# Performance work log

Hardware: AMD Instinct MI355X
Metric: run time of the kernel (lower is better)

## Reference

```python
import jax, jax.numpy as jnp
import numpy as np
from jax import lax

B, S, H, E, P, K, R = 64, 512, 768, 32, 16, 9, 6
HEADS, C1, C2 = 4, 128, 64
FEAT = 4 * C2 + 1  # e1, e2, e1*e2, context (64 each) + log-distance


def _ln(x, g, b):
    m = x.mean(-1, keepdims=True)
    v = ((x - m) ** 2).mean(-1, keepdims=True)
    return (x - m) * lax.rsqrt(v + 1e-5) * g + b


def _gat(x, adj, W, a_s, a_d, bias, heads, cout, concat):
    # Dense GATConv over a small fully-masked entity graph. adj[b,i,j]=edge j->i (incl. self-loops).
    h = jnp.einsum('bef,fhc->behc', x, W.reshape(x.shape[-1], heads, cout))
    s = jnp.einsum('behc,hc->bhe', h, a_s)  # source-node attention term
    d = jnp.einsum('behc,hc->bhe', h, a_d)  # target-node attention term
    logits = jax.nn.leaky_relu(d[:, :, :, None] + s[:, :, None, :], 0.2)  # [b,h,i,j]
    logits = jnp.where(adj[:, None, :, :], logits, -1e9)
    att = jax.nn.softmax(logits, axis=-1)
    out = jnp.einsum('bhij,bjhc->bihc', att, h)
    out = out.reshape(out.shape[0], out.shape[1], heads * cout) if concat else out.mean(2)
    return out + bias


def _crf_nll(em, tags, mask, start, end, trans):
    # torchcrf: loss = -mean log-likelihood. em [B,S,K]; tags [B,S]; mask [B,S] bool.
    emt = jnp.transpose(em, (1, 0, 2))
    tgt = tags.T
    mkt = mask.T.astype(em.dtype)
    num0 = start[tgt[0]] + jnp.take_along_axis(emt[0], tgt[0][:, None], 1)[:, 0]

    def nstep(c, inp):
        ptag, sc = c
        e, t, m = inp
        step = trans[ptag, t] + jnp.take_along_axis(e, t[:, None], 1)[:, 0]
        return (jnp.where(m > 0, t, ptag), sc + step * m), None

    (ltag, num), _ = lax.scan(nstep, (tgt[0], num0), (emt[1:], tgt[1:], mkt[1:]))
    num = num + end[ltag]
    a0 = start[None, :] + emt[0]

    def dstep(a, inp):
        e, m = inp
        nxt = jax.scipy.special.logsumexp(a[:, :, None] + trans[None] + e[:, None, :], axis=1)
        return jnp.where(m[:, None] > 0, nxt, a), None

    aT, _ = lax.scan(dstep, a0, (emt[1:], mkt[1:]))
    Z = jax.scipy.special.logsumexp(aT + end[None], axis=1)
    return jnp.mean(Z - num)


def setup_inputs() -> dict:
    key = jax.random.key(0)
    ks = jax.random.split(key, 24)
    n = lambda i, shape, s=0.05: jax.random.normal(ks[i], shape, jnp.float32) * s
    return {
        'sequence_output': jax.random.normal(ks[0], (B, S, H), jnp.float32),
        'attention_mask': jnp.ones((B, S), jnp.int32),
        'ner_labels': jax.random.randint(ks[1], (B, S), 0, K),
        'entity_start': jax.random.randint(ks[2], (B, E), 0, S - 8),
        'entity_len': jax.random.randint(ks[3], (B, E), 0, 8),
        'pair_e1': jax.random.randint(ks[4], (B, P), 0, E),
        'pair_e2': jax.random.randint(ks[5], (B, P), 0, E),
        'pair_labels': jax.random.randint(ks[6], (B, P), 0, 2),
        'adj_mask': jnp.ones((B, E, E), bool),
        'w_ner1': n(7, (H, 256)), 'b_ner1': jnp.zeros((256,), jnp.float32),
        'w_ner2': n(8, (256, K)), 'b_ner2': jnp.zeros((K,), jnp.float32),
        'crf_start': n(9, (K,), 0.1), 'crf_end': n(10, (K,), 0.1), 'crf_trans': n(11, (K, K), 0.1),
        'w_gat1': n(12, (H, HEADS * C1)), 'a_src1': n(13, (HEADS, C1)), 'a_dst1': n(14, (HEADS, C1)),
        'b_gat1': jnp.zeros((HEADS * C1,), jnp.float32),
        'w_gat2': n(15, (HEADS * C1, C2)), 'a_src2': n(16, (1, C2)), 'a_dst2': n(17, (1, C2)),
        'b_gat2': jnp.zeros((C2,), jnp.float32),
        'w_fe': n(18, (FEAT, 512)), 'b_fe': jnp.zeros((512,), jnp.float32),
        'g_fe': jnp.ones((512,), jnp.float32), 'be_fe': jnp.zeros((512,), jnp.float32),
        'w_rc1': n(19, (R, 512, 256)), 'b_rc1': jnp.zeros((R, 256), jnp.float32),
        'g_rc': jnp.ones((R, 256), jnp.float32), 'be_rc': jnp.zeros((R, 256), jnp.float32),
        'w_rc2': n(20, (R, 256, 1)), 'b_rc2': jnp.zeros((R,), jnp.float32),
    }


def reference(sequence_output, attention_mask, ner_labels, entity_start, entity_len,
              pair_e1, pair_e2, pair_labels, adj_mask,
              w_ner1, b_ner1, w_ner2, b_ner2, crf_start, crf_end, crf_trans,
              w_gat1, a_src1, a_dst1, b_gat1, w_gat2, a_src2, a_dst2, b_gat2,
              w_fe, b_fe, g_fe, be_fe, w_rc1, b_rc1, g_rc, be_rc, w_rc2, b_rc2):
    # NER head (dropout off / eval)
    ner_logits = jnp.maximum(sequence_output @ w_ner1 + b_ner1, 0.0) @ w_ner2 + b_ner2
    ner_loss = _crf_nll(ner_logits, ner_labels, attention_mask.astype(bool),
                        crf_start, crf_end, crf_trans)
    # entity span mean-pool via inclusive cumsum trick
    cs = jnp.concatenate([jnp.zeros((B, 1, H), sequence_output.dtype),
                          jnp.cumsum(sequence_output, axis=1)], axis=1)
    e_end = jnp.clip(entity_start + entity_len, 0, S - 1)
    seg = (jnp.take_along_axis(cs, (e_end + 1)[:, :, None], 1)
           - jnp.take_along_axis(cs, entity_start[:, :, None], 1))
    ent = seg / (e_end - entity_start + 1).astype(sequence_output.dtype)[:, :, None]  # [B,E,H]
    x = _gat(ent, adj_mask, w_gat1, a_src1, a_dst1, b_gat1, HEADS, C1, True)
    x = jnp.maximum(x, 0.0)
    x = _gat(x, adj_mask, w_gat2, a_src2, a_dst2, b_gat2, 1, C2, False)  # [B,E,64]
    x1 = jnp.take_along_axis(x, pair_e1[:, :, None], 1)
    x2 = jnp.take_along_axis(x, pair_e2[:, :, None], 1)
    ctx = jnp.broadcast_to(x.mean(1, keepdims=True), (B, P, C2))
    dist = jnp.log(jnp.abs(pair_e1 - pair_e2).astype(x.dtype) + 1.0)[:, :, None]
    pf = jnp.concatenate([x1, x2, x1 * x2, ctx, dist], axis=-1)  # [B,P,257]
    fe = jax.nn.leaky_relu(_ln(pf @ w_fe + b_fe, g_fe, be_fe), 0.01)
    h1 = jnp.einsum('bpf,rfo->rbpo', fe, w_rc1) + b_rc1[:, None, None, :]
    h1 = jax.nn.leaky_relu(_ln(h1, g_rc[:, None, None, :], be_rc[:, None, None, :]), 0.01)
    z = jnp.einsum('rbpo,ro->rbp', h1, w_rc2[:, :, 0]) + b_rc2[:, None, None]
    y = pair_labels.astype(z.dtype)[None]
    # BCEWithLogitsLoss(pos_weight=2.0), mean per relation type, summed over types
    bce = -(2.0 * y * jax.nn.log_sigmoid(z) + (1.0 - y) * jax.nn.log_sigmoid(-z))
    rel_loss = bce.mean(axis=(1, 2)).sum()
    total = ner_loss + rel_loss
    return ner_logits, z, total
```

## Files before the change

kernel.cpp:

```cpp
#include <hip/hip_runtime.h>
#include <math.h>


#define NB 64
#define NS 512
#define NH 768
#define NE 32
#define NP 16
#define NK 9
#define NR 6
#define NHEADS 4
#define NC1 128
#define NC2 64
#define SEGS 16
#define SEGLEN 32

#define ZOFF 294912
#define TOTOFF 301056

#define WS_ENT   0u
#define WS_X1    2621440u
#define WS_X2    3801088u
#define WS_PF    3956736u
#define WS_FE    4222976u
#define WS_CRF   4747264u
#define WS_REL   4747328u
#define WS_W1T   4747392u
#define WS_WRT   0u
#define WS_WFET  393216u
#define WS_SEG   475136u

typedef __attribute__((ext_vector_type(8))) short bf16x8;
typedef __attribute__((ext_vector_type(4))) float f32x4;

__device__ __forceinline__ unsigned short f2bf(float x) {
  union { float f; unsigned u; } v; v.f = x;
  unsigned r = v.u + 0x7FFFu + ((v.u >> 16) & 1u);
  return (unsigned short)(r >> 16);
}

__device__ __forceinline__ float logsigf(float x) {
  if (x >= 0.f) return -log1pf(__expf(-x));
  return x - log1pf(__expf(x));
}

__global__ __launch_bounds__(256) void k_w1t(const float* __restrict__ w1,
    unsigned short* __restrict__ w1t) {
  __shared__ unsigned short tr[32 * 776];
  const int c0 = blockIdx.x * 32;
  const int t = threadIdx.x;
#pragma unroll
  for (int p = 0; p < 24; p++) {
    const int k = p * 32 + (t >> 3), c4 = t & 7;
    const float4 f = *reinterpret_cast<const float4*>(&w1[(size_t)k * 256 + c0 + c4 * 4]);
    tr[(c4 * 4 + 0) * 776 + k] = f2bf(f.x);
    tr[(c4 * 4 + 1) * 776 + k] = f2bf(f.y);
    tr[(c4 * 4 + 2) * 776 + k] = f2bf(f.z);
    tr[(c4 * 4 + 3) * 776 + k] = f2bf(f.w);
  }
  __syncthreads();
  const int c = t >> 3, q = t & 7;
#pragma unroll
  for (int i = 0; i < 12; i++) {
    *reinterpret_cast<uint4*>(&w1t[(size_t)(c0 + c) * NH + q * 96 + i * 8]) =
        *reinterpret_cast<const uint4*>(&tr[c * 776 + q * 96 + i * 8]);
  }
}

__global__ __launch_bounds__(256) void k_wconv(const float* __restrict__ wrc,
    const float* __restrict__ wfe, unsigned short* __restrict__ wrt,
    unsigned short* __restrict__ wfet) {
  __shared__ unsigned short tr[256 * 72];
  const int t = threadIdx.x;
  if (blockIdx.x < 48) {
    const int r = blockIdx.x >> 3, kt = blockIdx.x & 7;
    const int k0 = kt * 64;
#pragma unroll
    for (int i = 0; i < 16; i++) {
      const int slot = t + 256 * i;
      const int row = slot >> 6, c4 = slot & 63;
      const float4 f = *reinterpret_cast<const float4*>(
          &wrc[((size_t)(r * 512) + k0 + row) * 256 + c4 * 4]);
      tr[(c4 * 4 + 0) * 72 + row] = f2bf(f.x);
      tr[(c4 * 4 + 1) * 72 + row] = f2bf(f.y);
      tr[(c4 * 4 + 2) * 72 + row] = f2bf(f.z);
      tr[(c4 * 4 + 3) * 72 + row] = f2bf(f.w);
    }
    __syncthreads();
#pragma unroll
    for (int i = 0; i < 8; i++) {
      const int slot = t + 256 * i;
      const int col = slot >> 3, q = slot & 7;
      *reinterpret_cast<uint4*>(&wrt[((size_t)(r * 256 + col)) * 512 + k0 + q * 8]) =
          *reinterpret_cast<const uint4*>(&tr[col * 72 + q * 8]);
    }
  } else {
    const int bid = blockIdx.x - 48;
    const int kt = bid % 5, cb = bid / 5;
    const int k0 = kt * 64, c0 = cb * 256;
#pragma unroll
    for (int i = 0; i < 16; i++) {
      const int slot = t + 256 * i;
      const int row = slot >> 6, c4 = slot & 63;
      const int k = k0 + row;
      float4 f = {0.f, 0.f, 0.f, 0.f};
      if (k < 257)
        f = *reinterpret_cast<const float4*>(&wfe[(size_t)k * 512 + c0 + c4 * 4]);
      tr[(c4 * 4 + 0) * 72 + row] = f2bf(f.x);
      tr[(c4 * 4 + 1) * 72 + row] = f2bf(f.y);
      tr[(c4 * 4 + 2) * 72 + row] = f2bf(f.z);
      tr[(c4 * 4 + 3) * 72 + row] = f2bf(f.w);
    }
    __syncthreads();
#pragma unroll
    for (int i = 0; i < 8; i++) {
      const int slot = t + 256 * i;
      const int col = slot >> 3, q = slot & 7;
      *reinterpret_cast<uint4*>(&wfet[((size_t)(c0 + col)) * 320 + k0 + q * 8]) =
          *reinterpret_cast<const uint4*>(&tr[col * 72 + q * 8]);
    }
  }
}

__global__ __launch_bounds__(256) void k_ner(const float* __restrict__ seq,
    const unsigned short* __restrict__ w1t, const float* __restrict__ b1,
    const float* __restrict__ w2, const float* __restrict__ b2,
    float* __restrict__ out) {
  __shared__ unsigned short AsS[64 * 40];
  __shared__ unsigned short BsS[256 * 40];
  __shared__ float zs[64 * 4 * 12];
  const int t = threadIdx.x;
  const int tok0 = blockIdx.x * 64;
  const int w = t >> 6, lane = t & 63, quad = lane >> 4, l15 = lane & 15;

  f32x4 acc[4][4];
#pragma unroll
  for (int r = 0; r < 4; r++)
#pragma unroll
    for (int c = 0; c < 4; c++) acc[r][c] = (f32x4){0.f, 0.f, 0.f, 0.f};

  const int tokA = t >> 2, koffA = (t & 3) * 8;
  const float* aptr = seq + (size_t)(tok0 + tokA) * NH + koffA;

  for (int kt = 0; kt < NH; kt += 32) {
    __syncthreads();
    {
      const float4 f0 = *reinterpret_cast<const float4*>(aptr + kt);
      const float4 f1 = *reinterpret_cast<const float4*>(aptr + kt + 4);
      bf16x8 av;
      av[0] = (short)f2bf(f0.x); av[1] = (short)f2bf(f0.y);
      av[2] = (short)f2bf(f0.z); av[3] = (short)f2bf(f0.w);
      av[4] = (short)f2bf(f1.x); av[5] = (short)f2bf(f1.y);
      av[6] = (short)f2bf(f1.z); av[7] = (short)f2bf(f1.w);
      *reinterpret_cast<bf16x8*>(&AsS[tokA * 40 + koffA]) = av;
    }
#pragma unroll
    for (int i = 0; i < 4; i++) {
      const int q = t + 256 * i;
      const int col = q >> 2, koff = (q & 3) * 8;
      *reinterpret_cast<uint4*>(&BsS[col * 40 + koff]) =
          *reinterpret_cast<const uint4*>(&w1t[(size_t)col * NH + kt + koff]);
    }
    __syncthreads();
    bf16x8 a[4], b[4];
#pragma unroll
    for (int r = 0; r < 4; r++)
      a[r] = *reinterpret_cast<const bf16x8*>(&AsS[(r * 16 + l15) * 40 + quad * 8]);
#pragma unroll
    for (int c = 0; c < 4; c++)
      b[c] = *reinterpret_cast<const bf16x8*>(&BsS[(w * 64 + c * 16 + l15) * 40 + quad * 8]);
#pragma unroll
    for (int r = 0; r < 4; r++)
#pragma unroll
      for (int c = 0; c < 4; c++)
        acc[r][c] = __builtin_amdgcn_mfma_f32_16x16x32_bf16(a[r], b[c], acc[r][c], 0, 0, 0);
  }

  float b1v[4], w2v[4][NK];
#pragma unroll
  for (int c = 0; c < 4; c++) {
    const int col = w * 64 + c * 16 + l15;
    b1v[c] = b1[col];
#pragma unroll
    for (int cc = 0; cc < NK; cc++) w2v[c][cc] = w2[col * NK + cc];
  }
#pragma unroll
  for (int r = 0; r < 4; r++) {
#pragma unroll
    for (int reg = 0; reg < 4; reg++) {
      float p[NK];
#pragma unroll
      for (int cc = 0; cc < NK; cc++) p[cc] = 0.f;
#pragma unroll
      for (int c = 0; c < 4; c++) {
        const float h = fmaxf(acc[r][c][reg] + b1v[c], 0.f);
#pragma unroll
        for (int cc = 0; cc < NK; cc++) p[cc] = fmaf(h, w2v[c][cc], p[cc]);
      }
#pragma unroll
      for (int o = 1; o < 16; o <<= 1)
#pragma unroll
        for (int cc = 0; cc < NK; cc++) p[cc] += __shfl_xor(p[cc], o);
      if (l15 == 0) {
        const int tokr = r * 16 + quad * 4 + reg;
#pragma unroll
        for (int cc = 0; cc < NK; cc++) zs[(tokr * 4 + w) * 12 + cc] = p[cc];
      }
    }
  }
  __syncthreads();
  if (t < 64) {
#pragma unroll
    for (int cc = 0; cc < NK; cc++) {
      const float z = zs[(t * 4 + 0) * 12 + cc] + zs[(t * 4 + 1) * 12 + cc] +
                      zs[(t * 4 + 2) * 12 + cc] + zs[(t * 4 + 3) * 12 + cc] + b2[cc];
      out[(size_t)(tok0 + t) * NK + cc] = z;
    }
  }
}

__global__ __launch_bounds__(128) void k_crf_seg(const float* __restrict__ em,
    const int* __restrict__ mask, const float* __restrict__ trans,
    float* __restrict__ segm) {
  __shared__ float bufA[16 * 81];
  __shared__ float bufB[8 * 81];
  __shared__ float ems[SEGLEN * 9];
  __shared__ int mks[SEGLEN];
  __shared__ float trs[81];
  const int blk = blockIdx.x;
  const int b = blk >> 4, seg = blk & 15;
  const int t = threadIdx.x;
  const int s0 = 1 + seg * SEGLEN;
  const float* emb = em + (size_t)b * NS * NK;
  const int* mk = mask + b * NS;
  if (t < 81) trs[t] = trans[t];
  for (int i = t; i < SEGLEN * 9; i += 128) {
    const int g = s0 * 9 + i;
    ems[i] = (g < NS * 9) ? emb[g] : 0.f;
  }
  if (t < SEGLEN) {
    const int s = s0 + t;
    mks[t] = (s < NS) ? mk[s] : 0;
  }
  __syncthreads();
  for (int idx = t; idx < 16 * 81; idx += 128) {
    const int p = idx / 81, e = idx % 81, i = e / 9, j = e % 9;
    const int la = 2 * p, lb = la + 1;
    const bool ma = mks[la] > 0, mb = mks[lb] > 0;
    float r;
    if (ma && mb) {
      float v[9], mx = -1e30f;
#pragma unroll
      for (int m = 0; m < 9; m++) {
        v[m] = trs[i * 9 + m] + ems[la * 9 + m] + trs[m * 9 + j];
        mx = fmaxf(mx, v[m]);
      }
      float sum = 0.f;
#pragma unroll
      for (int m = 0; m < 9; m++) sum += __expf(v[m] - mx);
      r = mx + __logf(sum) + ems[lb * 9 + j];
    } else if (ma) {
      r = trs[e] + ems[la * 9 + j];
    } else if (mb) {
      r = trs[e] + ems[lb * 9 + j];
    } else {
      r = (i == j) ? 0.f : -1e30f;
    }
    bufA[p * 81 + e] = r;
  }
  float* src = bufA;
  float* dst = bufB;
  for (int n = 16; n > 1; n >>= 1) {
    __syncthreads();
    const int half = n >> 1;
    for (int idx = t; idx < half * 81; idx += 128) {
      const int q = idx / 81, e = idx % 81, i = e / 9, j = e % 9;
      const float* A = src + (size_t)(2 * q) * 81;
      const float* Bm = src + (size_t)(2 * q + 1) * 81;
      float v[9], mx = -1e30f;
#pragma unroll
      for (int m = 0; m < 9; m++) {
        v[m] = A[i * 9 + m] + Bm[m * 9 + j];
        mx = fmaxf(mx, v[m]);
      }
      float sum = 0.f;
#pragma unroll
      for (int m = 0; m < 9; m++) sum += __expf(v[m] - mx);
      dst[q * 81 + e] = mx + __logf(sum);
    }
    float* tmp = src; src = dst; dst = tmp;
  }
  __syncthreads();
  if (t < 81) segm[((size_t)b * SEGS + seg) * 81 + t] = src[t];
}

__global__ __launch_bounds__(64) void k_crf_fin(const float* __restrict__ em,
    const int* __restrict__ tags, const int* __restrict__ mask,
    const float* __restrict__ startv, const float* __restrict__ endv,
    const float* __restrict__ trans, const float* __restrict__ segm,
    float* __restrict__ lossb) {
  __shared__ float sm[SEGS * 81];
  __shared__ float av[16];
  __shared__ float red[2];
  const int b = blockIdx.x, t = threadIdx.x;
  const float* emb = em + (size_t)b * NS * NK;
  const int* mk = mask + b * NS;
  const int* tg = tags + b * NS;
  for (int i = t; i < SEGS * 81; i += 64) sm[i] = segm[(size_t)b * SEGS * 81 + i];
  {
    float num = 0.f;
    int lastS = 0;
#pragma unroll
    for (int o = 0; o < 8; o++) {
      const int s = t * 8 + o;
      if (s >= 1 && mk[s] > 0) {
        const int cur = tg[s], prv = tg[s - 1];
        num += trans[prv * NK + cur] + emb[s * NK + cur];
        lastS = s;
      }
    }
#pragma unroll
    for (int o = 32; o > 0; o >>= 1) {
      num += __shfl_xor(num, o);
      lastS = max(lastS, __shfl_xor(lastS, o));
    }
    if (t == 0) {
      const int t0 = tg[0];
      red[0] = startv[t0] + emb[t0] + num + endv[tg[lastS]];
    }
  }
  __syncthreads();
  if (t < 9) av[t] = startv[t] + emb[t];
  __syncthreads();
  for (int h = 0; h < SEGS; h++) {
    float nv = 0.f;
    if (t < 9) {
      float v[9], mx = -1e30f;
#pragma unroll
      for (int i2 = 0; i2 < 9; i2++) {
        v[i2] = av[i2] + sm[h * 81 + i2 * 9 + t];
        mx = fmaxf(mx, v[i2]);
      }
      float sum = 0.f;
#pragma unroll
      for (int i2 = 0; i2 < 9; i2++) sum += __expf(v[i2] - mx);
      nv = mx + __logf(sum);
    }
    __syncthreads();
    if (t < 9) av[t] = nv;
    __syncthreads();
  }
  if (t == 0) {
    float mx = -1e30f;
#pragma unroll
    for (int j = 0; j < 9; j++) mx = fmaxf(mx, av[j] + endv[j]);
    float sum = 0.f;
#pragma unroll
    for (int j = 0; j < 9; j++) sum += __expf(av[j] + endv[j] - mx);
    lossb[b] = (mx + __logf(sum)) - red[0];
  }
}

__global__ __launch_bounds__(256) void k_ent(const float* __restrict__ seq,
    const int* __restrict__ est, const int* __restrict__ elen, float* __restrict__ ent) {
  const int be = blockIdx.x;
  const int b = be >> 5, e = be & 31;
  const int st = est[b * NE + e];
  int en = st + elen[b * NE + e];
  en = min(max(en, 0), NS - 1);
  const float inv = 1.f / (float)(en - st + 1);
  for (int c = threadIdx.x; c < NH; c += 256) {
    float s = 0.f;
    for (int r = st; r <= en; r++) s += seq[((size_t)b * NS + r) * NH + c];
    ent[((size_t)b * NE + e) * NH + c] = s * inv;
  }
}

__global__ __launch_bounds__(256) void k_g1f(const float* __restrict__ ent,
    const float* __restrict__ w, const float* __restrict__ as,
    const float* __restrict__ ad, const unsigned char* __restrict__ adj,
    const float* __restrict__ bias, float* __restrict__ x1) {
  __shared__ float As[32 * 36];
  __shared__ float Bs[32 * 128];
  __shared__ float Hs[32 * 132];
  __shared__ float Att[32 * 32];
  __shared__ float Sv[32], Dv[32];
  const int b = blockIdx.x >> 2, hd = blockIdx.x & 3;
  const int t = threadIdx.x;
  const int tc = t & 31, tr = t >> 5;
  float acc[4][4];
#pragma unroll
  for (int i = 0; i < 4; i++)
#pragma unroll
    for (int j = 0; j < 4; j++) acc[i][j] = 0.f;
  for (int kt = 0; kt < NH; kt += 32) {
    __syncthreads();
    {
      const int e = t >> 3, k4 = t & 7;
      *reinterpret_cast<float4*>(&As[e * 36 + k4 * 4]) =
          *reinterpret_cast<const float4*>(&ent[((size_t)b * NE + e) * NH + kt + k4 * 4]);
    }
#pragma unroll
    for (int i = 0; i < 4; i++) {
      const int slot = t + 256 * i;
      const int row = slot >> 5, cg = slot & 31;
      *reinterpret_cast<float4*>(&Bs[row * 128 + cg * 4]) =
          *reinterpret_cast<const float4*>(&w[(size_t)(kt + row) * 512 + hd * 128 + cg * 4]);
    }
    __syncthreads();
#pragma unroll
    for (int kg = 0; kg < 8; kg++) {
      float4 a[4];
#pragma unroll
      for (int i = 0; i < 4; i++)
        a[i] = *reinterpret_cast<const float4*>(&As[(tr * 4 + i) * 36 + kg * 4]);
#pragma unroll
      for (int k2 = 0; k2 < 4; k2++) {
        const float4 bv = *reinterpret_cast<const float4*>(&Bs[(kg * 4 + k2) * 128 + tc * 4]);
#pragma unroll
        for (int i = 0; i < 4; i++) {
          const float av = reinterpret_cast<const float*>(&a[i])[k2];
          acc[i][0] = fmaf(av, bv.x, acc[i][0]);
          acc[i][1] = fmaf(av, bv.y, acc[i][1]);
          acc[i][2] = fmaf(av, bv.z, acc[i][2]);
          acc[i][3] = fmaf(av, bv.w, acc[i][3]);
        }
      }
    }
  }
#pragma unroll
  for (int i = 0; i < 4; i++)
#pragma unroll
    for (int j = 0; j < 4; j++)
      Hs[(tr * 4 + i) * 132 + tc * 4 + j] = acc[i][j];
  __syncthreads();
  {
    const int e = t >> 3, cg = t & 7;
    float sv = 0.f, dv = 0.f;
#pragma unroll
    for (int c = 0; c < 16; c++) {
      const float h = Hs[e * 132 + cg * 16 + c];
      sv += h * as[hd * NC1 + cg * 16 + c];
      dv += h * ad[hd * NC1 + cg * 16 + c];
    }
#pragma unroll
    for (int o = 1; o < 8; o <<= 1) { sv += __shfl_xor(sv, o); dv += __shfl_xor(dv, o); }
    if (cg == 0) { Sv[e] = sv; Dv[e] = dv; }
  }
  __syncthreads();
  if (t < 32) {
    const int i = t;
    const float di = Dv[i];
    float lg[32];
    float m = -1e30f;
#pragma unroll
    for (int j = 0; j < 32; j++) {
      float v = di + Sv[j];
      v = v >= 0.f ? v : 0.2f * v;
      if (!adj[((size_t)b * NE + i) * NE + j]) v = -1e9f;
      lg[j] = v; m = fmaxf(m, v);
    }
    float sum = 0.f;
#pragma unroll
    for (int j = 0; j < 32; j++) { lg[j] = __expf(lg[j] - m); sum += lg[j]; }
    const float inv = 1.f / sum;
#pragma unroll
    for (int j = 0; j < 32; j++) Att[j * 32 + i] = lg[j] * inv;
  }
  __syncthreads();
#pragma unroll
  for (int i = 0; i < 4; i++) {
    const int row = tr * 4 + i;
    float o0 = bias[hd * NC1 + tc * 4 + 0];
    float o1 = bias[hd * NC1 + tc * 4 + 1];
    float o2 = bias[hd * NC1 + tc * 4 + 2];
    float o3 = bias[hd * NC1 + tc * 4 + 3];
#pragma unroll
    for (int j = 0; j < 32; j++) {
      const float a = Att[j * 32 + row];
      o0 = fmaf(a, Hs[j * 132 + tc * 4 + 0], o0);
      o1 = fmaf(a, Hs[j * 132 + tc * 4 + 1], o1);
      o2 = fmaf(a, Hs[j * 132 + tc * 4 + 2], o2);
      o3 = fmaf(a, Hs[j * 132 + tc * 4 + 3], o3);
    }
    float4 v;
    v.x = fmaxf(o0, 0.f); v.y = fmaxf(o1, 0.f);
    v.z = fmaxf(o2, 0.f); v.w = fmaxf(o3, 0.f);
    *reinterpret_cast<float4*>(&x1[((size_t)b * NE + row) * 512 + hd * 128 + tc * 4]) = v;
  }
}

__global__ __launch_bounds__(256) void k_g2f(const float* __restrict__ x1,
    const float* __restrict__ w, const float* __restrict__ as,
    const float* __restrict__ ad, const unsigned char* __restrict__ adj,
    const float* __restrict__ bias, float* __restrict__ x2) {
  __shared__ float As[32 * 36];
  __shared__ float Bs[32 * 64];
  __shared__ float H2[32 * 68];
  __shared__ float Att[32 * 32];
  __shared__ float Sv[32], Dv[32];
  const int b = blockIdx.x;
  const int t = threadIdx.x;
  const int tc = t & 15, tr = t >> 4;
  float acc[2][4];
#pragma unroll
  for (int i = 0; i < 2; i++)
#pragma unroll
    for (int j = 0; j < 4; j++) acc[i][j] = 0.f;
  for (int kt = 0; kt < 512; kt += 32) {
    __syncthreads();
    {
      const int e = t >> 3, k4 = t & 7;
      *reinterpret_cast<float4*>(&As[e * 36 + k4 * 4]) =
          *reinterpret_cast<const float4*>(&x1[((size_t)b * NE + e) * 512 + kt + k4 * 4]);
    }
#pragma unroll
    for (int i = 0; i < 2; i++) {
      const int slot = t + 256 * i;
      const int row = slot >> 4, cg = slot & 15;
      *reinterpret_cast<float4*>(&Bs[row * 64 + cg * 4]) =
          *reinterpret_cast<const float4*>(&w[(size_t)(kt + row) * NC2 + cg * 4]);
    }
    __syncthreads();
#pragma unroll
    for (int kg = 0; kg < 8; kg++) {
      float4 a[2];
#pragma unroll
      for (int i = 0; i < 2; i++)
        a[i] = *reinterpret_cast<const float4*>(&As[(tr * 2 + i) * 36 + kg * 4]);
#pragma unroll
      for (int k2 = 0; k2 < 4; k2++) {
        const float4 bv = *reinterpret_cast<const float4*>(&Bs[(kg * 4 + k2) * 64 + tc * 4]);
#pragma unroll
        for (int i = 0; i < 2; i++) {
          const float av = reinterpret_cast<const float*>(&a[i])[k2];
          acc[i][0] = fmaf(av, bv.x, acc[i][0]);
          acc[i][1] = fmaf(av, bv.y, acc[i][1]);
          acc[i][2] = fmaf(av, bv.z, acc[i][2]);
          acc[i][3] = fmaf(av, bv.w, acc[i][3]);
        }
      }
    }
  }
  const float4 a4s = *reinterpret_cast<const float4*>(&as[tc * 4]);
  const float4 a4d = *reinterpret_cast<const float4*>(&ad[tc * 4]);
#pragma unroll
  for (int i = 0; i < 2; i++) {
    const int e = tr * 2 + i;
    float4 v;
    v.x = acc[i][0]; v.y = acc[i][1]; v.z = acc[i][2]; v.w = acc[i][3];
    *reinterpret_cast<float4*>(&H2[e * 68 + tc * 4]) = v;
    float sv = v.x * a4s.x + v.y * a4s.y + v.z * a4s.z + v.w * a4s.w;
    float dv = v.x * a4d.x + v.y * a4d.y + v.z * a4d.z + v.w * a4d.w;
#pragma unroll
    for (int o = 8; o > 0; o >>= 1) { sv += __shfl_xor(sv, o); dv += __shfl_xor(dv, o); }
    if (tc == 0) { Sv[e] = sv; Dv[e] = dv; }
  }
  __syncthreads();
  if (t < 32) {
    const int i = t;
    const float di = Dv[i];
    float lg[32];
    float m = -1e30f;
#pragma unroll
    for (int j = 0; j < 32; j++) {
      float v = di + Sv[j];
      v = v >= 0.f ? v : 0.2f * v;
      if (!adj[((size_t)b * NE + i) * NE + j]) v = -1e9f;
      lg[j] = v; m = fmaxf(m, v);
    }
    float sum = 0.f;
#pragma unroll
    for (int j = 0; j < 32; j++) { lg[j] = __expf(lg[j] - m); sum += lg[j]; }
    const float inv = 1.f / sum;
#pragma unroll
    for (int j = 0; j < 32; j++) Att[j * 32 + i] = lg[j] * inv;
  }
  __syncthreads();
#pragma unroll
  for (int i = 0; i < 2; i++) {
    const int row = tr * 2 + i;
    float o0 = bias[tc * 4 + 0];
    float o1 = bias[tc * 4 + 1];
    float o2 = bias[tc * 4 + 2];
    float o3 = bias[tc * 4 + 3];
#pragma unroll
    for (int j = 0; j < 32; j++) {
      const float a = Att[j * 32 + row];
      o0 = fmaf(a, H2[j * 68 + tc * 4 + 0], o0);
      o1 = fmaf(a, H2[j * 68 + tc * 4 + 1], o1);
      o2 = fmaf(a, H2[j * 68 + tc * 4 + 2], o2);
      o3 = fmaf(a, H2[j * 68 + tc * 4 + 3], o3);
    }
    float4 v;
    v.x = o0; v.y = o1; v.z = o2; v.w = o3;
    *reinterpret_cast<float4*>(&x2[((size_t)b * NE + row) * NC2 + tc * 4]) = v;
  }
}

__global__ __launch_bounds__(64) void k_pf(const float* __restrict__ x2,
    const int* __restrict__ pe1, const int* __restrict__ pe2,
    float* __restrict__ pf) {
  const int bp = blockIdx.x;
  const int b = bp >> 4, p = bp & 15;
  const int t = threadIdx.x;
  const int e1 = pe1[b * NP + p], e2 = pe2[b * NP + p];
  const float v1 = x2[((size_t)b * NE + e1) * NC2 + t];
  const float v2 = x2[((size_t)b * NE + e2) * NC2 + t];
  float cs = 0.f;
  for (int e = 0; e < NE; e++) cs += x2[((size_t)b * NE + e) * NC2 + t];
  float* row = pf + (size_t)bp * 260;
  row[t] = v1;
  row[64 + t] = v2;
  row[128 + t] = v1 * v2;
  row[192 + t] = cs * (1.f / NE);
  if (t == 0) row[256] = logf(fabsf((float)(e1 - e2)) + 1.f);
  if (t < 3) row[257 + t] = 0.f;
}

__global__ __launch_bounds__(256) void k_fe(const float* __restrict__ pf,
    const unsigned short* __restrict__ wt, const float* __restrict__ bfe,
    const float* __restrict__ g, const float* __restrict__ be,
    unsigned short* __restrict__ feb) {
  __shared__ unsigned short Af[16 * 320];
  __shared__ float Cs[16 * 520];
  const int b = blockIdx.x, t = threadIdx.x;
  const int w = t >> 6, lane = t & 63, quad = lane >> 4, l15 = lane & 15;
  for (int i = t; i < 16 * 320; i += 256) {
    const int p = i / 320, k = i - p * 320;
    Af[i] = (k < 260) ? f2bf(pf[(size_t)(b * NP + p) * 260 + k]) : (unsigned short)0;
  }
  __syncthreads();
  f32x4 acc[8];
#pragma unroll
  for (int c = 0; c < 8; c++) acc[c] = (f32x4){0.f, 0.f, 0.f, 0.f};
#pragma unroll
  for (int kt = 0; kt < 10; kt++) {
    const bf16x8 a = *reinterpret_cast<const bf16x8*>(&Af[l15 * 320 + kt * 32 + quad * 8]);
#pragma unroll
    for (int c = 0; c < 8; c++) {
      const int col = w * 128 + c * 16 + l15;
      const bf16x8 bv = *reinterpret_cast<const bf16x8*>(&wt[(size_t)col * 320 + kt * 32 + quad * 8]);
      acc[c] = __builtin_amdgcn_mfma_f32_16x16x32_bf16(a, bv, acc[c], 0, 0, 0);
    }
  }
#pragma unroll
  for (int c = 0; c < 8; c++)
#pragma unroll
    for (int reg = 0; reg < 4; reg++)
      Cs[(quad * 4 + reg) * 520 + w * 128 + c * 16 + l15] = acc[c][reg];
  __syncthreads();
  float bfev[8], gv[8], bev[8];
#pragma unroll
  for (int ch = 0; ch < 8; ch++) {
    const int col = ch * 64 + lane;
    bfev[ch] = bfe[col]; gv[ch] = g[col]; bev[ch] = be[col];
  }
#pragma unroll
  for (int pp = 0; pp < 4; pp++) {
    const int p = w * 4 + pp;
    float v[8], s = 0.f, sq = 0.f;
#pragma unroll
    for (int ch = 0; ch < 8; ch++) {
      v[ch] = Cs[p * 520 + ch * 64 + lane] + bfev[ch];
      s += v[ch]; sq += v[ch] * v[ch];
    }
#pragma unroll
    for (int o = 32; o > 0; o >>= 1) { s += __shfl_xor(s, o); sq += __shfl_xor(sq, o); }
    const float mean = s * (1.f / 512.f);
    const float var = sq * (1.f / 512.f) - mean * mean;
    const float rr = rsqrtf(var + 1e-5f);
#pragma unroll
    for (int ch = 0; ch < 8; ch++) {
      float n = (v[ch] - mean) * rr * gv[ch] + bev[ch];
      n = n >= 0.f ? n : 0.01f * n;
      feb[(size_t)(b * NP + p) * 512 + ch * 64 + lane] = f2bf(n);
    }
  }
}

__global__ __launch_bounds__(256) void k_rc(const unsigned short* __restrict__ feb,
    const unsigned short* __restrict__ wrt, const float* __restrict__ b1,
    const float* __restrict__ g, const float* __restrict__ be,
    const float* __restrict__ w2, const float* __restrict__ b2,
    const int* __restrict__ ylab, float* __restrict__ zout, float* __restrict__ relacc) {
  __shared__ unsigned short Af[16 * 520];
  __shared__ float Cs[16 * 264];
  const int blk = blockIdx.x;
  const int r = blk >> 6, b = blk & 63;
  const int t = threadIdx.x;
  const int w = t >> 6, lane = t & 63, quad = lane >> 4, l15 = lane & 15;
#pragma unroll
  for (int i = 0; i < 4; i++) {
    const int slot = t + 256 * i;
    const int p = slot >> 6, q = slot & 63;
    *reinterpret_cast<uint4*>(&Af[p * 520 + q * 8]) =
        *reinterpret_cast<const uint4*>(&feb[(size_t)(b * NP + p) * 512 + q * 8]);
  }
  __syncthreads();
  f32x4 acc[4];
#pragma unroll
  for (int c = 0; c < 4; c++) acc[c] = (f32x4){0.f, 0.f, 0.f, 0.f};
#pragma unroll
  for (int kt = 0; kt < 16; kt++) {
    const bf16x8 a = *reinterpret_cast<const bf16x8*>(&Af[l15 * 520 + kt * 32 + quad * 8]);
#pragma unroll
    for (int c = 0; c < 4; c++) {
      const int col = w * 64 + c * 16 + l15;
      const bf16x8 bv = *reinterpret_cast<const bf16x8*>(
          &wrt[(size_t)(r * 256 + col) * 512 + kt * 32 + quad * 8]);
      acc[c] = __builtin_amdgcn_mfma_f32_16x16x32_bf16(a, bv, acc[c], 0, 0, 0);
    }
  }
#pragma unroll
  for (int c = 0; c < 4; c++)
#pragma unroll
    for (int reg = 0; reg < 4; reg++)
      Cs[(quad * 4 + reg) * 264 + w * 64 + c * 16 + l15] = acc[c][reg];
  __syncthreads();
  float b1v[4], gv[4], bev[4], w2v[4];
#pragma unroll
  for (int ch = 0; ch < 4; ch++) {
    const int col = r * 256 + ch * 64 + lane;
    b1v[ch] = b1[col]; gv[ch] = g[col]; bev[ch] = be[col]; w2v[ch] = w2[col];
  }
  const float b2v = b2[r];
  float local = 0.f;
#pragma unroll
  for (int pp = 0; pp < 4; pp++) {
    const int p = w * 4 + pp;
    float v[4], s = 0.f, sq = 0.f;
#pragma unroll
    for (int ch = 0; ch < 4; ch++) {
      v[ch] = Cs[p * 264 + ch * 64 + lane] + b1v[ch];
      s += v[ch]; sq += v[ch] * v[ch];
    }
#pragma unroll
    for (int o = 32; o > 0; o >>= 1) { s += __shfl_xor(s, o); sq += __shfl_xor(sq, o); }
    const float mean = s * (1.f / 256.f);
    const float var = sq * (1.f / 256.f) - mean * mean;
    const float rr = rsqrtf(var + 1e-5f);
    float zdot = 0.f;
#pragma unroll
    for (int ch = 0; ch < 4; ch++) {
      float n = (v[ch] - mean) * rr * gv[ch] + bev[ch];
      n = n >= 0.f ? n : 0.01f * n;
      zdot = fmaf(n, w2v[ch], zdot);
    }
#pragma unroll
    for (int o = 32; o > 0; o >>= 1) zdot += __shfl_xor(zdot, o);
    if (lane == 0) {
      const float zp = zdot + b2v;
      zout[(size_t)(r * NB + b) * NP + p] = zp;
      const float y = (float)ylab[b * NP + p];
      local += -(2.f * y * logsigf(zp) + (1.f - y) * logsigf(-zp));
    }
  }
  if (lane == 0) atomicAdd(relacc, local * (1.f / (NB * NP)));
}

__global__ __launch_bounds__(64) void k_fin(const float* __restrict__ lossb,
    const float* __restrict__ rel, float* __restrict__ out) {
  float v = lossb[threadIdx.x];
#pragma unroll
  for (int o = 32; o > 0; o >>= 1) v += __shfl_down(v, o);
  if (threadIdx.x == 0) out[TOTOFF] = v * (1.f / NB) + rel[0];
}

extern "C" void kernel_launch(void* const* d_in, const int* in_sizes, int n_in,
                              void* d_out, int out_size, void* d_ws, size_t ws_size,
                              hipStream_t stream) {
  const float* seq = (const float*)d_in[0];
  const int* amask = (const int*)d_in[1];
  const int* nlab = (const int*)d_in[2];
  const int* est = (const int*)d_in[3];
  const int* elen = (const int*)d_in[4];
  const int* pe1 = (const int*)d_in[5];
  const int* pe2 = (const int*)d_in[6];
  const int* plab = (const int*)d_in[7];
  const unsigned char* adj = (const unsigned char*)d_in[8];
  const float* w_ner1 = (const float*)d_in[9];
  const float* b_ner1 = (const float*)d_in[10];
  const float* w_ner2 = (const float*)d_in[11];
  const float* b_ner2 = (const float*)d_in[12];
  const float* crf_start = (const float*)d_in[13];
  const float* crf_end = (const float*)d_in[14];
  const float* crf_trans = (const float*)d_in[15];
  const float* w_gat1 = (const float*)d_in[16];
  const float* a_src1 = (const float*)d_in[17];
  const float* a_dst1 = (const float*)d_in[18];
  const float* b_gat1 = (const float*)d_in[19];
  const float* w_gat2 = (const float*)d_in[20];
  const float* a_src2 = (const float*)d_in[21];
  const float* a_dst2 = (const float*)d_in[22];
  const float* b_gat2 = (const float*)d_in[23];
  const float* w_fe = (const float*)d_in[24];
  const float* b_fe = (const float*)d_in[25];
  const float* g_fe = (const float*)d_in[26];
  const float* be_fe = (const float*)d_in[27];
  const float* w_rc1 = (const float*)d_in[28];
  const float* b_rc1 = (const float*)d_in[29];
  const float* g_rc = (const float*)d_in[30];
  const float* be_rc = (const float*)d_in[31];
  const float* w_rc2 = (const float*)d_in[32];
  const float* b_rc2 = (const float*)d_in[33];

  float* out = (float*)d_out;
  float* ws = (float*)d_ws;
  float* ent = ws + WS_ENT;
  float* x1 = ws + WS_X1;
  float* x2 = ws + WS_X2;
  float* pf = ws + WS_PF;
  float* crfb = ws + WS_CRF;
  float* rel = ws + WS_REL;
  unsigned short* w1t = (unsigned short*)(ws + WS_W1T);
  unsigned short* feb = (unsigned short*)(ws + WS_FE);
  unsigned short* wrt = (unsigned short*)(ws + WS_WRT);
  unsigned short* wfet = (unsigned short*)(ws + WS_WFET);
  float* segm = ws + WS_SEG;

  hipMemsetAsync(rel, 0, sizeof(float), stream);

  k_w1t<<<8, 256, 0, stream>>>(w_ner1, w1t);
  k_ner<<<512, 256, 0, stream>>>(seq, w1t, b_ner1, w_ner2, b_ner2, out);
  k_ent<<<NB * NE, 256, 0, stream>>>(seq, est, elen, ent);
  k_g1f<<<NB * NHEADS, 256, 0, stream>>>(ent, w_gat1, a_src1, a_dst1, adj, b_gat1, x1);
  k_wconv<<<58, 256, 0, stream>>>(w_rc1, w_fe, wrt, wfet);
  k_crf_seg<<<NB * SEGS, 128, 0, stream>>>(out, amask, crf_trans, segm);
  k_crf_fin<<<NB, 64, 0, stream>>>(out, nlab, amask, crf_start, crf_end, crf_trans,
                                   segm, crfb);
  k_g2f<<<NB, 256, 0, stream>>>(x1, w_gat2, a_src2, a_dst2, adj, b_gat2, x2);
  k_pf<<<NB * NP, 64, 0, stream>>>(x2, pe1, pe2, pf);
  k_fe<<<NB, 256, 0, stream>>>(pf, wfet, b_fe, g_fe, be_fe, feb);
  k_rc<<<NR * NB, 256, 0, stream>>>(feb, wrt, b_rc1, g_rc, be_rc, w_rc2, b_rc2,
                                    plab, out + ZOFF, rel);
  k_fin<<<1, 64, 0, stream>>>(crfb, rel, out);
}
```

Measured before the change: 472.4 us.

## Use bf16 MFMA for GAT layer-1 projection with pre-transposed weights

The first GAT projection moves from an fp32 FMA tiled GEMM to bf16 MFMA 16x16x32. Entity means are stored as bf16 and the GAT1 weight is transposed and converted to bf16 in the existing weight-transpose kernel, which now runs extra blocks. This cuts FMA work and global traffic for the per-batch, per-head projection. It costs precision from bf16 rounding of the inputs and weights.

```diff
diff --git a/kernel.cpp b/kernel.cpp
--- a/kernel.cpp
+++ b/kernel.cpp
@@ -19,6 +19,7 @@
 #define TOTOFF 301056
 
 #define WS_ENT   0u
+#define WS_WG1T  1572864u
 #define WS_X1    2621440u
 #define WS_X2    3801088u
 #define WS_PF    3956736u
@@ -44,15 +45,20 @@
   return x - log1pf(__expf(x));
 }
 
-__global__ __launch_bounds__(256) void k_w1t(const float* __restrict__ w1,
-    unsigned short* __restrict__ w1t) {
+__global__ __launch_bounds__(256) void k_wt(const float* __restrict__ w1,
+    const float* __restrict__ wg1, unsigned short* __restrict__ w1t,
+    unsigned short* __restrict__ wg1t) {
   __shared__ unsigned short tr[32 * 776];
-  const int c0 = blockIdx.x * 32;
   const int t = threadIdx.x;
+  const float* src;
+  unsigned short* dst;
+  int c0, ncol;
+  if (blockIdx.x < 8) { src = w1; dst = w1t; ncol = 256; c0 = blockIdx.x * 32; }
+  else { src = wg1; dst = wg1t; ncol = 512; c0 = (blockIdx.x - 8) * 32; }
 #pragma unroll
   for (int p = 0; p < 24; p++) {
     const int k = p * 32 + (t >> 3), c4 = t & 7;
-    const float4 f = *reinterpret_cast<const float4*>(&w1[(size_t)k * 256 + c0 + c4 * 4]);
+    const float4 f = *reinterpret_cast<const float4*>(&src[(size_t)k * ncol + c0 + c4 * 4]);
     tr[(c4 * 4 + 0) * 776 + k] = f2bf(f.x);
     tr[(c4 * 4 + 1) * 776 + k] = f2bf(f.y);
     tr[(c4 * 4 + 2) * 776 + k] = f2bf(f.z);
@@ -62,7 +68,7 @@
   const int c = t >> 3, q = t & 7;
 #pragma unroll
   for (int i = 0; i < 12; i++) {
-    *reinterpret_cast<uint4*>(&w1t[(size_t)(c0 + c) * NH + q * 96 + i * 8]) =
+    *reinterpret_cast<uint4*>(&dst[(size_t)(c0 + c) * NH + q * 96 + i * 8]) =
         *reinterpret_cast<const uint4*>(&tr[c * 776 + q * 96 + i * 8]);
   }
 }
@@ -362,7 +368,8 @@
 }
 
 __global__ __launch_bounds__(256) void k_ent(const float* __restrict__ seq,
-    const int* __restrict__ est, const int* __restrict__ elen, float* __restrict__ ent) {
+    const int* __restrict__ est, const int* __restrict__ elen,
+    unsigned short* __restrict__ entb) {
   const int be = blockIdx.x;
   const int b = be >> 5, e = be & 31;
   const int st = est[b * NE + e];
@@ -372,67 +379,66 @@
   for (int c = threadIdx.x; c < NH; c += 256) {
     float s = 0.f;
     for (int r = st; r <= en; r++) s += seq[((size_t)b * NS + r) * NH + c];
-    ent[((size_t)b * NE + e) * NH + c] = s * inv;
-  }
-}
-
-__global__ __launch_bounds__(256) void k_g1f(const float* __restrict__ ent,
-    const float* __restrict__ w, const float* __restrict__ as,
+    entb[((size_t)b * NE + e) * NH + c] = f2bf(s * inv);
+  }
+}
+
+__global__ __launch_bounds__(256) void k_g1f(const unsigned short* __restrict__ entb,
+    const unsigned short* __restrict__ wg1t, const float* __restrict__ as,
     const float* __restrict__ ad, const unsigned char* __restrict__ adj,
     const float* __restrict__ bias, float* __restrict__ x1) {
-  __shared__ float As[32 * 36];
-  __shared__ float Bs[32 * 128];
+  __shared__ unsigned short As[32 * 40];
+  __shared__ unsigned short Bs[128 * 40];
   __shared__ float Hs[32 * 132];
   __shared__ float Att[32 * 32];
   __shared__ float Sv[32], Dv[32];
   const int b = blockIdx.x >> 2, hd = blockIdx.x & 3;
   const int t = threadIdx.x;
-  const int tc = t & 31, tr = t >> 5;
-  float acc[4][4];
-#pragma unroll
-  for (int i = 0; i < 4; i++)
-#pragma unroll
-    for (int j = 0; j < 4; j++) acc[i][j] = 0.f;
+  const int w = t >> 6, lane = t & 63, quad = lane >> 4, l15 = lane & 15;
+
+  f32x4 acc[2][2];
+#pragma unroll
+  for (int r = 0; r < 2; r++)
+#pragma unroll
+    for (int c = 0; c < 2; c++) acc[r][c] = (f32x4){0.f, 0.f, 0.f, 0.f};
+
+  const int rowA = t >> 2, koffA = (t & 3) * 8;
+  const unsigned short* aptr = entb + ((size_t)(b * NE) + rowA) * NH + koffA;
+
   for (int kt = 0; kt < NH; kt += 32) {
     __syncthreads();
-    {
-      const int e = t >> 3, k4 = t & 7;
-      *reinterpret_cast<float4*>(&As[e * 36 + k4 * 4]) =
-          *reinterpret_cast<const float4*>(&ent[((size_t)b * NE + e) * NH + kt + k4 * 4]);
-    }
-#pragma unroll
-    for (int i = 0; i < 4; i++) {
-      const int slot = t + 256 * i;
-      const int row = slot >> 5, cg = slot & 31;
-      *reinterpret_cast<float4*>(&Bs[row * 128 + cg * 4]) =
-          *reinterpret_cast<const float4*>(&w[(size_t)(kt + row) * 512 + hd * 128 + cg * 4]);
-    }
-    __syncthreads();
-#pragma unroll
-    for (int kg = 0; kg < 8; kg++) {
-      float4 a[4];
-#pragma unroll
-      for (int i = 0; i < 4; i++)
-        a[i] = *reinterpret_cast<const float4*>(&As[(tr * 4 + i) * 36 + kg * 4]);
-#pragma unroll
-      for (int k2 = 0; k2 < 4; k2++) {
-        const float4 bv = *reinterpret_cast<const float4*>(&Bs[(kg * 4 + k2) * 128 + tc * 4]);
-#pragma unroll
-        for (int i = 0; i < 4; i++) {
-          const float av = reinterpret_cast<const float*>(&a[i])[k2];
-          acc[i][0] = fmaf(av, bv.x, acc[i][0]);
-          acc[i][1] = fmaf(av, bv.y, acc[i][1]);
-          acc[i][2] = fmaf(av, bv.z, acc[i][2]);
-          acc[i][3] = fmaf(av, bv.w, acc[i][3]);
-        }
-      }
-    }
-  }
-#pragma unroll
-  for (int i = 0; i < 4; i++)
-#pragma unroll
-    for (int j = 0; j < 4; j++)
-      Hs[(tr * 4 + i) * 132 + tc * 4 + j] = acc[i][j];
+    if (t < 128) {
+      *reinterpret_cast<uint4*>(&As[rowA * 40 + koffA]) =
+          *reinterpret_cast<const uint4*>(aptr + kt);
+    }
+#pragma unroll
+    for (int i = 0; i < 2; i++) {
+      const int q = t + 256 * i;
+      const int col = q >> 2, koff = (q & 3) * 8;
+      *reinterpret_cast<uint4*>(&Bs[col * 40 + koff]) =
+          *reinterpret_cast<const uint4*>(&wg1t[(size_t)(hd * 128 + col) * NH + kt + koff]);
+    }
+    __syncthreads();
+    bf16x8 a[2], bb[2];
+#pragma unroll
+    for (int r = 0; r < 2; r++)
+      a[r] = *reinterpret_cast<const bf16x8*>(&As[(r * 16 + l15) * 40 + quad * 8]);
+#pragma unroll
+    for (int c = 0; c < 2; c++)
+      bb[c] = *reinterpret_cast<const bf16x8*>(&Bs[(w * 32 + c * 16 + l15) * 40 + quad * 8]);
+#pragma unroll
+    for (int r = 0; r < 2; r++)
+#pragma unroll
+      for (int c = 0; c < 2; c++)
+        acc[r][c] = __builtin_amdgcn_mfma_f32_16x16x32_bf16(a[r], bb[c], acc[r][c], 0, 0, 0);
+  }
+#pragma unroll
+  for (int r = 0; r < 2; r++)
+#pragma unroll
+    for (int c = 0; c < 2; c++)
+#pragma unroll
+      for (int reg = 0; reg < 4; reg++)
+        Hs[(r * 16 + quad * 4 + reg) * 132 + w * 32 + c * 16 + l15] = acc[r][c][reg];
   __syncthreads();
   {
     const int e = t >> 3, cg = t & 7;
@@ -468,25 +474,28 @@
     for (int j = 0; j < 32; j++) Att[j * 32 + i] = lg[j] * inv;
   }
   __syncthreads();
-#pragma unroll
-  for (int i = 0; i < 4; i++) {
-    const int row = tr * 4 + i;
-    float o0 = bias[hd * NC1 + tc * 4 + 0];
-    float o1 = bias[hd * NC1 + tc * 4 + 1];
-    float o2 = bias[hd * NC1 + tc * 4 + 2];
-    float o3 = bias[hd * NC1 + tc * 4 + 3];
-#pragma unroll
-    for (int j = 0; j < 32; j++) {
-      const float a = Att[j * 32 + row];
-      o0 = fmaf(a, Hs[j * 132 + tc * 4 + 0], o0);
-      o1 = fmaf(a, Hs[j * 132 + tc * 4 + 1], o1);
-      o2 = fmaf(a, Hs[j * 132 + tc * 4 + 2], o2);
-      o3 = fmaf(a, Hs[j * 132 + tc * 4 + 3], o3);
-    }
-    float4 v;
-    v.x = fmaxf(o0, 0.f); v.y = fmaxf(o1, 0.f);
-    v.z = fmaxf(o2, 0.f); v.w = fmaxf(o3, 0.f);
-    *reinterpret_cast<float4*>(&x1[((size_t)b * NE + row) * 512 + hd * 128 + tc * 4]) = v;
+  {
+    const int tc = t & 31, tr = t >> 5;
+#pragma unroll
+    for (int i = 0; i < 4; i++) {
+      const int row = tr * 4 + i;
+      float o0 = bias[hd * NC1 + tc * 4 + 0];
+      float o1 = bias[hd * NC1 + tc * 4 + 1];
+      float o2 = bias[hd * NC1 + tc * 4 + 2];
+      float o3 = bias[hd * NC1 + tc * 4 + 3];
+#pragma unroll
+      for (int j = 0; j < 32; j++) {
+        const float a = Att[j * 32 + row];
+        o0 = fmaf(a, Hs[j * 132 + tc * 4 + 0], o0);
+        o1 = fmaf(a, Hs[j * 132 + tc * 4 + 1], o1);
+        o2 = fmaf(a, Hs[j * 132 + tc * 4 + 2], o2);
+        o3 = fmaf(a, Hs[j * 132 + tc * 4 + 3], o3);
+      }
+      float4 v;
+      v.x = fmaxf(o0, 0.f); v.y = fmaxf(o1, 0.f);
+      v.z = fmaxf(o2, 0.f); v.w = fmaxf(o3, 0.f);
+      *reinterpret_cast<float4*>(&x1[((size_t)b * NE + row) * 512 + hd * 128 + tc * 4]) = v;
+    }
   }
 }
 
@@ -807,12 +816,13 @@
 
   float* out = (float*)d_out;
   float* ws = (float*)d_ws;
-  float* ent = ws + WS_ENT;
   float* x1 = ws + WS_X1;
   float* x2 = ws + WS_X2;
   float* pf = ws + WS_PF;
   float* crfb = ws + WS_CRF;
   float* rel = ws + WS_REL;
+  unsigned short* entb = (unsigned short*)(ws + WS_ENT);
+  unsigned short* wg1t = (unsigned short*)(ws + WS_WG1T);
   unsigned short* w1t = (unsigned short*)(ws + WS_W1T);
   unsigned short* feb = (unsigned short*)(ws + WS_FE);
   unsigned short* wrt = (unsigned short*)(ws + WS_WRT);
@@ -821,10 +831,10 @@
 
   hipMemsetAsync(rel, 0, sizeof(float), stream);
 
-  k_w1t<<<8, 256, 0, stream>>>(w_ner1, w1t);
+  k_wt<<<24, 256, 0, stream>>>(w_ner1, w_gat1, w1t, wg1t);
   k_ner<<<512, 256, 0, stream>>>(seq, w1t, b_ner1, w_ner2, b_ner2, out);
-  k_ent<<<NB * NE, 256, 0, stream>>>(seq, est, elen, ent);
-  k_g1f<<<NB * NHEADS, 256, 0, stream>>>(ent, w_gat1, a_src1, a_dst1, adj, b_gat1, x1);
+  k_ent<<<NB * NE, 256, 0, stream>>>(seq, est, elen, entb);
+  k_g1f<<<NB * NHEADS, 256, 0, stream>>>(entb, wg1t, a_src1, a_dst1, adj, b_gat1, x1);
   k_wconv<<<58, 256, 0, stream>>>(w_rc1, w_fe, wrt, wfet);
   k_crf_seg<<<NB * SEGS, 128, 0, stream>>>(out, amask, crf_trans, segm);
   k_crf_fin<<<NB, 64, 0, stream>>>(out, nlab, amask, crf_start, crf_end, crf_trans,
```

After: 452.0 us. 1.05x faster.
